# Kernel optimization log

Measured on AMD Instinct MI355X. Metric: run time of the kernel, lower is better.

Reference implementation:

```python
import jax, jax.numpy as jnp
import numpy as np

NB, C, N, H, W = 2, 128, 4, 64, 64
K = 9  # 3x3 kernel positions


def _conv(x, w, b, pad):
    y = jax.lax.conv_general_dilated(x, w, (1, 1), ((pad, pad), (pad, pad)),
                                     dimension_numbers=('NCHW', 'OIHW', 'NCHW'))
    return y + b[None, :, None, None]


def _bn(x, g, be, m, v, eps=1e-5):
    scale = g / jnp.sqrt(v + eps)
    return x * scale[None, :, None, None] + (be - m * scale)[None, :, None, None]


def _maxpool(x):
    # MaxPool2d(kernel_size=2, stride=1, padding=1): output H+1, W+1
    return jax.lax.reduce_window(x, -jnp.inf, jax.lax.max, (1, 1, 2, 2), (1, 1, 1, 1),
                                 ((0, 0), (0, 0), (1, 1), (1, 1)))


def _deform_conv(x, offset, mask, w, b):
    # modulated deformable conv v2, kernel 3x3, stride 1, padding 1
    n, c, h, wd = x.shape
    ky = jnp.repeat(jnp.arange(3), 3).astype(x.dtype)  # kernel row offsets
    kx = jnp.tile(jnp.arange(3), 3).astype(x.dtype)    # kernel col offsets
    dy = offset[:, 0::2]  # [n,K,h,w] (torchvision layout: interleaved dy,dx)
    dx = offset[:, 1::2]
    py = jnp.arange(h, dtype=x.dtype)[None, None, :, None] - 1.0 + ky[None, :, None, None] + dy
    px = jnp.arange(wd, dtype=x.dtype)[None, None, None, :] - 1.0 + kx[None, :, None, None] + dx
    y0 = jnp.floor(py)
    x0 = jnp.floor(px)
    wy = py - y0
    wx = px - x0
    xt = jnp.transpose(x, (0, 2, 3, 1))  # [n,h,w,c]
    bidx = jnp.arange(n)[:, None, None, None]

    def gather(yi, xi):
        valid = ((yi >= 0) & (yi < h) & (xi >= 0) & (xi < wd)).astype(x.dtype)
        yc = jnp.clip(yi, 0, h - 1).astype(jnp.int32)
        xc = jnp.clip(xi, 0, wd - 1).astype(jnp.int32)
        return xt[bidx, yc, xc] * valid[..., None]  # [n,K,h,w,c]

    v = (((1 - wy) * (1 - wx))[..., None] * gather(y0, x0)
         + ((1 - wy) * wx)[..., None] * gather(y0, x0 + 1)
         + (wy * (1 - wx))[..., None] * gather(y0 + 1, x0)
         + (wy * wx)[..., None] * gather(y0 + 1, x0 + 1))
    v = v * mask[..., None]  # modulation mask [n,K,h,w]
    out = jnp.einsum('nkhwc,ock->nohw', v, w.reshape(w.shape[0], c, K))
    return out + b[None, :, None, None]


def _forward(x, w1, b1, g1, be1, m1, v1, w_off, b_off, w_mod, b_mod, w_def, b_def,
             g2, be2, m2, v2, w_ds, b_ds, g3, be3, m3, v3):
    for i in range(NB):
        h = jax.nn.relu(_bn(_conv(x, w1[i], b1[i], 1), g1[i], be1[i], m1[i], v1[i]))
        off = _conv(h, w_off[i], b_off[i], 1)
        msk = 2.0 * jax.nn.sigmoid(_conv(h, w_mod[i], b_mod[i], 1))
        d = _bn(_deform_conv(h, off, msk, w_def[i], b_def[i]), g2[i], be2[i], m2[i], v2[i])
        res = _bn(_conv(x, w_ds[i], b_ds[i], 0), g3[i], be3[i], m3[i], v3[i])
        x = _maxpool(jax.nn.relu(d + res))
    return x


def setup_inputs() -> dict:
    key = jax.random.key(0)
    ks = iter(jax.random.split(key, 48))

    def rn(shape, s=0.05):
        return jax.random.normal(next(ks), shape, jnp.float32) * s

    def bnp():
        g = jax.random.uniform(next(ks), (NB, C), jnp.float32) * 0.5 + 0.75
        be = rn((NB, C), 0.1)
        m = rn((NB, C), 0.1)
        v = jax.random.uniform(next(ks), (NB, C), jnp.float32) * 0.5 + 0.75
        return g, be, m, v

    g1, be1, m1, v1 = bnp()
    g2, be2, m2, v2 = bnp()
    g3, be3, m3, v3 = bnp()
    return dict(
        x=jax.random.normal(next(ks), (N, C, H, W), jnp.float32),
        w1=rn((NB, C, C, 3, 3)), b1=rn((NB, C)),
        g1=g1, be1=be1, m1=m1, v1=v1,
        w_off=rn((NB, 2 * K, C, 3, 3), 0.01), b_off=rn((NB, 2 * K), 0.01),
        w_mod=rn((NB, K, C, 3, 3), 0.01), b_mod=rn((NB, K), 0.01),
        w_def=rn((NB, C, C, 3, 3)), b_def=rn((NB, C)),
        g2=g2, be2=be2, m2=m2, v2=v2,
        w_ds=rn((NB, C, C, 1, 1)), b_ds=rn((NB, C)),
        g3=g3, be3=be3, m3=m3, v3=v3,
    )


def reference(x, w1, b1, g1, be1, m1, v1, w_off, b_off, w_mod, b_mod, w_def, b_def,
              g2, be2, m2, v2, w_ds, b_ds, g3, be3, m3, v3):
    return _forward(x, w1, b1, g1, be1, m1, v1, w_off, b_off, w_mod, b_mod, w_def, b_def,
                    g2, be2, m2, v2, w_ds, b_ds, g3, be3, m3, v3)
```

## Files before the change

kernel.cpp:

```cpp
#include <hip/hip_runtime.h>
#include <math.h>

constexpr int NN = 4;
constexpr int CC = 128;

typedef unsigned short u16;
typedef short bfrag __attribute__((ext_vector_type(8)));
typedef float facc  __attribute__((ext_vector_type(4)));

__device__ __forceinline__ float bf2f(u16 v) {
    unsigned u = ((unsigned)v) << 16; float f; __builtin_memcpy(&f, &u, 4); return f;
}
__device__ __forceinline__ u16 f2bf(float f) {
    unsigned u; __builtin_memcpy(&u, &f, 4);
    unsigned r = u + 0x7FFFu + ((u >> 16) & 1u);
    return (u16)(r >> 16);
}

typedef const __attribute__((address_space(1))) unsigned int gu32;
typedef __attribute__((address_space(3))) unsigned int lu32;
__device__ __forceinline__ void gload16(const u16* g, u16* l) {
    __builtin_amdgcn_global_load_lds((gu32*)g, (lu32*)l, 16, 0, 0);
}

template<int WM, int WN, int MR, int NR, int NOB, int EPI>
__global__ __launch_bounds__(512)
void gconv_h(const u16* __restrict__ A, const u16* __restrict__ Wp,
             const float* __restrict__ bias, void* __restrict__ Out,
             int H, int W, int npb)
{
    constexpr int HALOW = 68;
    __shared__ __align__(16) u16 halo[4 * HALOW * 128];

    const int Hp = H + 2, Wq = W + 2, HW = H * W;
    const int tid = threadIdx.x, lane = tid & 63, wv = tid >> 6;
    const int wn = wv % WN, wm = wv / WN;
    const int colc = lane & 15, kg = lane >> 4;
    const int n = blockIdx.x / npb;
    const int pib = (blockIdx.x - n * npb) * 64;
    const int ymin = pib / W;

    {
        const u16* Abase = A + (size_t)n * Hp * Wq * 128;
        for (int c = wv; c < 4 * HALOW / 4; c += 8) {
            int o = c * 512 + lane * 8;
            int r = o / (HALOW * 128);
            int e = o - r * (HALOW * 128);
            int x = e >> 7;
            int g = (e >> 3) & 15;
            int xs = x < Wq ? x : Wq - 1;
            int pr = ymin + r; if (pr > Hp - 1) pr = Hp - 1;
            const u16* src = Abase + ((size_t)pr * Wq + xs) * 128 + (g ^ (x & 7)) * 8;
            gload16(src, &halo[c * 512]);
        }
    }
    __syncthreads();

    int dyr[MR], axr[MR];
#pragma unroll
    for (int r = 0; r < MR; ++r) {
        int m = wm * (MR * 16) + r * 16 + colc;
        int pixl = pib + m; if (pixl > HW - 1) pixl = HW - 1;
        int y = pixl / W;
        dyr[r] = y - ymin; axr[r] = pixl - y * W;
    }

    auto wfrag = [&](int tap, int cc, int q) -> const bfrag* {
        return (const bfrag*)(Wp + (size_t)tap * (NOB * 2048)
                              + ((cc * NOB + wn * NR + q) * 64 + lane) * 8);
    };

    bfrag bc[4][NR];
#pragma unroll
    for (int cc = 0; cc < 4; ++cc)
#pragma unroll
        for (int q = 0; q < NR; ++q) bc[cc][q] = *wfrag(0, cc, q);

    facc acc[MR][NR];
#pragma unroll
    for (int r = 0; r < MR; ++r)
#pragma unroll
        for (int q = 0; q < NR; ++q) acc[r][q] = (facc){0.f, 0.f, 0.f, 0.f};

#pragma unroll 1
    for (int t = 0; t < 9; ++t) {
        int ty = t / 3, tx = t - ty * 3;
        bfrag bn_[4][NR];
        if (t < 8) {
#pragma unroll
            for (int cc = 0; cc < 4; ++cc)
#pragma unroll
                for (int q = 0; q < NR; ++q) bn_[cc][q] = *wfrag(t + 1, cc, q);
        }
#pragma unroll
        for (int cc = 0; cc < 4; ++cc) {
            bfrag a[MR];
#pragma unroll
            for (int r = 0; r < MR; ++r) {
                int xx = axr[r] + tx;
                a[r] = *(const bfrag*)&halo[((dyr[r] + ty) * HALOW + xx) * 128
                                            + ((cc * 4 + kg) ^ (xx & 7)) * 8];
            }
#pragma unroll
            for (int r = 0; r < MR; ++r)
#pragma unroll
                for (int q = 0; q < NR; ++q)
                    acc[r][q] = __builtin_amdgcn_mfma_f32_16x16x32_bf16(a[r], bc[cc][q], acc[r][q], 0, 0, 0);
        }
        if (t < 8) {
#pragma unroll
            for (int cc = 0; cc < 4; ++cc)
#pragma unroll
                for (int q = 0; q < NR; ++q) bc[cc][q] = bn_[cc][q];
        }
    }

#pragma unroll
    for (int r = 0; r < MR; ++r) {
#pragma unroll
        for (int j = 0; j < 4; ++j) {
            int m = wm * (MR * 16) + r * 16 + kg * 4 + j;
            int pixl = pib + m;
            if (pixl >= HW) continue;
#pragma unroll
            for (int q = 0; q < NR; ++q) {
                int oc = wn * (NR * 16) + q * 16 + colc;
                float val = acc[r][q][j] + bias[oc];
                if constexpr (EPI == 0) {
                    val = fmaxf(val, 0.f);
                    int y = pixl / W, x = pixl - y * W;
                    ((u16*)Out)[((size_t)(n * Hp + y + 1) * Wq + x + 1) * 128 + oc] = f2bf(val);
                } else {
                    if (oc >= 18) val = 2.f / (1.f + expf(-val));
                    ((float*)Out)[((size_t)n * HW + pixl) * 32 + oc] = val;
                }
            }
        }
    }
}

__global__ __launch_bounds__(512, 4)
void deform7_k(const u16* __restrict__ Hb, const u16* __restrict__ Xp,
               const float* __restrict__ OM, const u16* __restrict__ Wp,
               const float* __restrict__ biasC, float* __restrict__ T,
               int H, int W, int tw, int th)
{
    __shared__ __align__(16) u16 halo[96 * 16 * 8];
    __shared__ __align__(16) u16 As3[3 * 32 * 128];
    __shared__ __align__(16) float oml[27 * 32];

    const int Hp = H + 2, Wq = W + 2, HW = H * W;
    const int tid = threadIdx.x, lane = tid & 63, wv = tid >> 6;
    const int wn = wv & 3, wm = wv >> 2;
    const int colc = lane & 15, kg = lane >> 4;
    int bt = blockIdx.x;
    int n = bt / (tw * th); int rt = bt - n * (tw * th);
    int ty0 = (rt / tw) * 4, tx0 = (rt - (rt / tw) * tw) * 8;
    const u16* Hbase = Hb + (size_t)n * Hp * Wq * 128;

#pragma unroll
    for (int c = 0; c < 3; ++c) {
        int g = c * 512 + tid;
        int s = g >> 4, u = g & 15;
        int row = s / 12, col = s - row * 12;
        int gy = min(max(ty0 - 2 + row, 0), H - 1);
        int gx = min(max(tx0 - 2 + col, 0), W - 1);
        int gr = u ^ (s & 15);
        gload16(Hbase + ((size_t)(gy + 1) * Wq + gx + 1) * 128 + gr * 8,
                &halo[(c * 512 + wv * 64) * 8]);
    }
    for (int e = tid; e < 27 * 32; e += 512) {
        int f = e >> 5, p = e & 31;
        int yy = min(ty0 + (p >> 3), H - 1), xx = min(tx0 + (p & 7), W - 1);
        oml[e] = OM[((size_t)n * HW + yy * W + xx) * 32 + f];
    }
    __syncthreads();

    const int g0 = tid & 15, m0 = (tid >> 4) & 31;
    const int cy1 = min(ty0 + (m0 >> 3), H - 1), cx1 = min(tx0 + (m0 & 7), W - 1);
    const int dslot = (g0 ^ (m0 & 7)) * 8;

    const int m = wm * 16 + colc;
    const int cyp = min(ty0 + (m >> 3), H - 1), cxp = min(tx0 + (m & 7), W - 1);
    const size_t xoff = ((size_t)(n * Hp + cyp + 1) * Wq + cxp + 1) * 128;

    auto wfrag = [&](int tap, int cc, int q) -> const bfrag* {
        return (const bfrag*)(Wp + (size_t)tap * 16384
                              + ((cc * 8 + wn * 2 + q) * 64 + lane) * 8);
    };

    auto sample1 = [&](int t, int tb) {
        float dy = oml[(2 * t) * 32 + m0];
        float dx = oml[(2 * t + 1) * 32 + m0];
        float mm = oml[(18 + t) * 32 + m0];
        float pyf = (float)cy1 - 1.f + (float)(t / 3) + dy;
        float pxf = (float)cx1 - 1.f + (float)(t % 3) + dx;
        float fy = floorf(pyf), fx = floorf(pxf);
        int y0 = (int)fy, x0 = (int)fx;
        float wy = pyf - fy, wx = pxf - fx;
        bool y0v = (y0 >= 0) && (y0 < H), y1v = (y0 >= -1) && (y0 < H - 1);
        bool x0v = (x0 >= 0) && (x0 < W), x1v = (x0 >= -1) && (x0 < W - 1);
        int yc0 = min(max(y0, 0), H - 1), yc1 = min(max(y0 + 1, 0), H - 1);
        int xc0 = min(max(x0, 0), W - 1), xc1 = min(max(x0 + 1, 0), W - 1);
        float w00 = (1.f - wy) * (1.f - wx) * ((y0v && x0v) ? mm : 0.f);
        float w01 = (1.f - wy) * wx         * ((y0v && x1v) ? mm : 0.f);
        float w10 = wy * (1.f - wx)         * ((y1v && x0v) ? mm : 0.f);
        float w11 = wy * wx                 * ((y1v && x1v) ? mm : 0.f);
        int ry0 = yc0 - ty0 + 2, ry1 = yc1 - ty0 + 2;
        int rx0 = xc0 - tx0 + 2, rx1 = xc1 - tx0 + 2;
        bool allin = (unsigned)ry0 < 8u && (unsigned)ry1 < 8u
                  && (unsigned)rx0 < 12u && (unsigned)rx1 < 12u;
        bfrag c00, c01, c10, c11;
        if (allin) {
            int s00 = ry0 * 12 + rx0, s01 = ry0 * 12 + rx1;
            int s10 = ry1 * 12 + rx0, s11 = ry1 * 12 + rx1;
            c00 = *(const bfrag*)&halo[(s00 * 16 + (g0 ^ (s00 & 15))) * 8];
            c01 = *(const bfrag*)&halo[(s01 * 16 + (g0 ^ (s01 & 15))) * 8];
            c10 = *(const bfrag*)&halo[(s10 * 16 + (g0 ^ (s10 & 15))) * 8];
            c11 = *(const bfrag*)&halo[(s11 * 16 + (g0 ^ (s11 & 15))) * 8];
        } else {
            c00 = *(const bfrag*)(Hbase + ((size_t)(yc0 + 1) * Wq + xc0 + 1) * 128 + g0 * 8);
            c01 = *(const bfrag*)(Hbase + ((size_t)(yc0 + 1) * Wq + xc1 + 1) * 128 + g0 * 8);
            c10 = *(const bfrag*)(Hbase + ((size_t)(yc1 + 1) * Wq + xc0 + 1) * 128 + g0 * 8);
            c11 = *(const bfrag*)(Hbase + ((size_t)(yc1 + 1) * Wq + xc1 + 1) * 128 + g0 * 8);
        }
        bfrag o;
#pragma unroll
        for (int j = 0; j < 8; ++j) {
            float f = w00 * bf2f((u16)c00[j]) + w01 * bf2f((u16)c01[j])
                    + w10 * bf2f((u16)c10[j]) + w11 * bf2f((u16)c11[j]);
            o[j] = (short)f2bf(f);
        }
        *(bfrag*)&As3[tb * 4096 + m0 * 128 + dslot] = o;
    };

    bfrag bc[4][2];
#pragma unroll
    for (int cc = 0; cc < 4; ++cc)
#pragma unroll
        for (int q = 0; q < 2; ++q) bc[cc][q] = *wfrag(0, cc, q);

    facc acc[2];
    acc[0] = (facc){0.f, 0.f, 0.f, 0.f};
    acc[1] = (facc){0.f, 0.f, 0.f, 0.f};

#pragma unroll 1
    for (int tg = 0; tg < 3; ++tg) {
        sample1(tg * 3 + 0, 0);
        sample1(tg * 3 + 1, 1);
        sample1(tg * 3 + 2, 2);
        __syncthreads();
#pragma unroll
        for (int tb = 0; tb < 3; ++tb) {
            int t = tg * 3 + tb;
            bfrag bn_[4][2];
#pragma unroll
            for (int cc = 0; cc < 4; ++cc)
#pragma unroll
                for (int q = 0; q < 2; ++q) bn_[cc][q] = *wfrag(t + 1, cc, q);
            const u16* as = &As3[tb * 4096];
#pragma unroll
            for (int cc = 0; cc < 4; ++cc) {
                bfrag a = *(const bfrag*)&as[m * 128 + ((cc * 4 + kg) ^ (m & 7)) * 8];
#pragma unroll
                for (int q = 0; q < 2; ++q)
                    acc[q] = __builtin_amdgcn_mfma_f32_16x16x32_bf16(a, bc[cc][q], acc[q], 0, 0, 0);
            }
#pragma unroll
            for (int cc = 0; cc < 4; ++cc)
#pragma unroll
                for (int q = 0; q < 2; ++q) bc[cc][q] = bn_[cc][q];
        }
        __syncthreads();
    }

#pragma unroll
    for (int cc = 0; cc < 4; ++cc) {
        bfrag a = *(const bfrag*)(Xp + xoff + (cc * 4 + kg) * 8);
#pragma unroll
        for (int q = 0; q < 2; ++q)
            acc[q] = __builtin_amdgcn_mfma_f32_16x16x32_bf16(a, bc[cc][q], acc[q], 0, 0, 0);
    }

#pragma unroll
    for (int j = 0; j < 4; ++j) {
        int mo = wm * 16 + kg * 4 + j;
        int y = ty0 + (mo >> 3), x = tx0 + (mo & 7);
        if (y >= H || x >= W) continue;
#pragma unroll
        for (int q = 0; q < 2; ++q) {
            int oc = wn * 32 + q * 16 + colc;
            T[((size_t)n * HW + y * W + x) * 128 + oc] = fmaxf(acc[q][j] + biasC[oc], 0.f);
        }
    }
}

template<int OUTMODE>
__global__ __launch_bounds__(256)
void pool_k(const float* __restrict__ T, void* __restrict__ Out, int H, int W)
{
    const int HW = H * W, Ho = H + 1, Wo = W + 1;
    int tot = NN * Ho * Wo * 16;
    int idx = blockIdx.x * 256 + threadIdx.x;
    if (idx >= tot) return;
    int cg = idx & 15; int t = idx >> 4;
    int ox = t % Wo; t /= Wo; int oy = t % Ho; int n = t / Ho;

    float mx[8];
#pragma unroll
    for (int j = 0; j < 8; ++j) mx[j] = -INFINITY;
#pragma unroll
    for (int d = 0; d < 2; ++d) {
        int iy = oy - 1 + d;
        if (iy < 0 || iy >= H) continue;
#pragma unroll
        for (int e = 0; e < 2; ++e) {
            int ix = ox - 1 + e;
            if (ix < 0 || ix >= W) continue;
            const float* src = T + ((size_t)(n * HW + iy * W + ix)) * 128 + cg * 8;
#pragma unroll
            for (int j = 0; j < 8; ++j) mx[j] = fmaxf(mx[j], src[j]);
        }
    }
    if constexpr (OUTMODE == 0) {
        int Hp2 = Ho + 2, Wp2 = Wo + 2;
        bfrag o;
#pragma unroll
        for (int j = 0; j < 8; ++j) o[j] = (short)f2bf(mx[j]);
        *(bfrag*)((u16*)Out + ((size_t)(n * Hp2 + oy + 1) * Wp2 + (ox + 1)) * 128 + cg * 8) = o;
    } else {
#pragma unroll
        for (int j = 0; j < 8; ++j) {
            int c = cg * 8 + j;
            ((float*)Out)[(((size_t)n * 128 + c) * Ho + oy) * Wo + ox] = mx[j];
        }
    }
}

__global__ __launch_bounds__(256)
void prolog_k(const float* __restrict__ x0,
              u16* __restrict__ Xp0, u16* __restrict__ Xp1,
              u16* __restrict__ Hp0, u16* __restrict__ Hp1,
              const float* __restrict__ w1, const float* __restrict__ b1,
              const float* __restrict__ g1, const float* __restrict__ be1,
              const float* __restrict__ m1, const float* __restrict__ v1,
              const float* __restrict__ w_off, const float* __restrict__ b_off,
              const float* __restrict__ w_mod, const float* __restrict__ b_mod,
              const float* __restrict__ w_def, const float* __restrict__ b_def,
              const float* __restrict__ g2, const float* __restrict__ be2,
              const float* __restrict__ m2, const float* __restrict__ v2,
              const float* __restrict__ w_ds, const float* __restrict__ b_ds,
              const float* __restrict__ g3, const float* __restrict__ be3,
              const float* __restrict__ m3, const float* __restrict__ v3,
              u16* __restrict__ Wb1p, u16* __restrict__ Wbomp, u16* __restrict__ Wbdp,
              float* __restrict__ bias1f, float* __restrict__ biasOM, float* __restrict__ biasC)
{
    const int P0 = 260, P1 = 264;
    const int B0 = NN * P0 * 16, B1 = NN * P1 * 16;
    int idx = blockIdx.x * 256 + threadIdx.x;
    bfrag z = (bfrag){0, 0, 0, 0, 0, 0, 0, 0};

    if (idx < 2 * B0) {
        u16* buf = idx < B0 ? Xp0 : Hp0;
        int e = idx < B0 ? idx : idx - B0;
        int gr = e & 15; int t = e >> 4;
        int b = t % P0; int n = t / P0;
        int y, x;
        if (b < 66)        { y = 0;  x = b; }
        else if (b < 132)  { y = 65; x = b - 66; }
        else { int r2 = b - 132; y = 1 + (r2 >> 1); x = (r2 & 1) ? 65 : 0; }
        *(bfrag*)(buf + ((size_t)(n * 66 + y) * 66 + x) * 128 + gr * 8) = z;
        return;
    }
    idx -= 2 * B0;
    if (idx < 2 * B1) {
        u16* buf = idx < B1 ? Xp1 : Hp1;
        int e = idx < B1 ? idx : idx - B1;
        int gr = e & 15; int t = e >> 4;
        int b = t % P1; int n = t / P1;
        int y, x;
        if (b < 67)        { y = 0;  x = b; }
        else if (b < 134)  { y = 66; x = b - 67; }
        else { int r2 = b - 134; y = 1 + (r2 >> 1); x = (r2 & 1) ? 66 : 0; }
        *(bfrag*)(buf + ((size_t)(n * 67 + y) * 67 + x) * 128 + gr * 8) = z;
        return;
    }
    idx -= 2 * B1;

    if (idx < NN * 64 * 64 * 16) {
        int cg = idx & 15; int t = idx >> 4;
        int x = t & 63; t >>= 6; int y = t & 63; int n = t >> 6;
        bfrag o;
#pragma unroll
        for (int j = 0; j < 8; ++j) {
            int c = cg * 8 + j;
            o[j] = (short)f2bf(x0[(((size_t)n * 128 + c) * 64 + y) * 64 + x]);
        }
        *(bfrag*)(Xp0 + ((size_t)(n * 66 + y + 1) * 66 + (x + 1)) * 128 + cg * 8) = o;
        return;
    }
    idx -= NN * 64 * 64 * 16;

    const int C1 = 9 * 4 * 8 * 512;
    const int C2 = 9 * 4 * 2 * 512;
    const int C3 = 10 * 4 * 8 * 512;
    if (idx < 2 * C1) {
        int inst = idx / C1, e = idx - inst * C1;
        int j = e & 7, lane = (e >> 3) & 63, rest = e >> 9;
        int ob = rest & 7; rest >>= 3; int cc = rest & 3; int tap = rest >> 2;
        int oc = ob * 16 + (lane & 15), c = cc * 32 + (lane >> 4) * 8 + j;
        float sc = g1[inst * 128 + oc] * rsqrtf(v1[inst * 128 + oc] + 1e-5f);
        Wb1p[idx] = f2bf(sc * w1[(((size_t)inst * 128 + oc) * 128 + c) * 9 + tap]);
        return;
    }
    idx -= 2 * C1;
    if (idx < 2 * C2) {
        int inst = idx / C2, e = idx - inst * C2;
        int j = e & 7, lane = (e >> 3) & 63, rest = e >> 9;
        int ob = rest & 1; rest >>= 1; int cc = rest & 3; int tap = rest >> 2;
        int oc = ob * 16 + (lane & 15), c = cc * 32 + (lane >> 4) * 8 + j;
        float v = 0.f;
        if (oc < 18)      v = w_off[(((size_t)inst * 18 + oc) * 128 + c) * 9 + tap];
        else if (oc < 27) v = w_mod[(((size_t)inst * 9 + (oc - 18)) * 128 + c) * 9 + tap];
        Wbomp[inst * C2 + e] = f2bf(v);
        return;
    }
    idx -= 2 * C2;
    if (idx < 2 * C3) {
        int inst = idx / C3, e = idx - inst * C3;
        int j = e & 7, lane = (e >> 3) & 63, rest = e >> 9;
        int ob = rest & 7; rest >>= 3; int cc = rest & 3; int tap = rest >> 2;
        int oc = ob * 16 + (lane & 15), c = cc * 32 + (lane >> 4) * 8 + j;
        float val;
        if (tap < 9) {
            float sc2 = g2[inst * 128 + oc] * rsqrtf(v2[inst * 128 + oc] + 1e-5f);
            val = sc2 * w_def[(((size_t)inst * 128 + oc) * 128 + c) * 9 + tap];
        } else {
            float sc3 = g3[inst * 128 + oc] * rsqrtf(v3[inst * 128 + oc] + 1e-5f);
            val = sc3 * w_ds[((size_t)inst * 128 + oc) * 128 + c];
        }
        Wbdp[inst * C3 + e] = f2bf(val);
        return;
    }
    idx -= 2 * C3;
    if (idx < 2 * 288) {
        int inst = idx / 288, r = idx - inst * 288;
        if (r < 128) {
            int oc = r, o = inst * 128 + oc;
            float sc = g1[o] * rsqrtf(v1[o] + 1e-5f);
            bias1f[o] = sc * b1[o] + be1[o] - m1[o] * sc;
        } else if (r < 160) {
            int oc = r - 128;
            float v = 0.f;
            if (oc < 18)      v = b_off[inst * 18 + oc];
            else if (oc < 27) v = b_mod[inst * 9 + (oc - 18)];
            biasOM[inst * 32 + oc] = v;
        } else {
            int oc = r - 160, o = inst * 128 + oc;
            float sc2 = g2[o] * rsqrtf(v2[o] + 1e-5f);
            float sc3 = g3[o] * rsqrtf(v3[o] + 1e-5f);
            biasC[o] = sc2 * b_def[o] + (be2[o] - m2[o] * sc2)
                     + sc3 * b_ds[o] + (be3[o] - m3[o] * sc3);
        }
    }
}

extern "C" void kernel_launch(void* const* d_in, const int* in_sizes, int n_in,
                              void* d_out, int out_size, void* d_ws, size_t ws_size,
                              hipStream_t stream)
{
    const float* x0    = (const float*)d_in[0];
    const float* w1    = (const float*)d_in[1];
    const float* b1    = (const float*)d_in[2];
    const float* g1    = (const float*)d_in[3];
    const float* be1   = (const float*)d_in[4];
    const float* m1    = (const float*)d_in[5];
    const float* v1    = (const float*)d_in[6];
    const float* w_off = (const float*)d_in[7];
    const float* b_off = (const float*)d_in[8];
    const float* w_mod = (const float*)d_in[9];
    const float* b_mod = (const float*)d_in[10];
    const float* w_def = (const float*)d_in[11];
    const float* b_def = (const float*)d_in[12];
    const float* g2    = (const float*)d_in[13];
    const float* be2   = (const float*)d_in[14];
    const float* m2    = (const float*)d_in[15];
    const float* v2    = (const float*)d_in[16];
    const float* w_ds  = (const float*)d_in[17];
    const float* b_ds  = (const float*)d_in[18];
    const float* g3    = (const float*)d_in[19];
    const float* be3   = (const float*)d_in[20];
    const float* m3    = (const float*)d_in[21];
    const float* v3    = (const float*)d_in[22];

    const int C1 = 147456, C2 = 36864, C3 = 163840;
    char* wsp = (char*)d_ws;
    auto alloc = [&](size_t bytes) { char* r = wsp; wsp += (bytes + 255) & ~(size_t)255; return r; };
    const size_t szX0 = (size_t)NN * 66 * 66 * 128 * 2;
    const size_t szX1 = (size_t)NN * 67 * 67 * 128 * 2;
    u16*   Xpad0  = (u16*)alloc(szX0);
    u16*   Xpad1  = (u16*)alloc(szX1);
    u16*   Hpad0  = (u16*)alloc(szX0);
    u16*   Hpad1  = (u16*)alloc(szX1);
    float* OFFMSK = (float*)alloc((size_t)16900 * 32 * 4);
    float* T      = (float*)alloc((size_t)16900 * 128 * 4);
    u16*   Wb1p   = (u16*)alloc((size_t)2 * C1 * 2);
    u16*   Wbomp  = (u16*)alloc((size_t)2 * C2 * 2);
    u16*   Wbdp   = (u16*)alloc((size_t)2 * C3 * 2);
    float* bias1f = (float*)alloc(2 * 128 * 4);
    float* biasOM = (float*)alloc(2 * 32 * 4);
    float* biasC  = (float*)alloc(2 * 128 * 4);

    const int B0 = NN * 260 * 16, B1 = NN * 264 * 16;
    int ptot = 2 * B0 + 2 * B1 + NN * 64 * 64 * 16 + 2 * C1 + 2 * C2 + 2 * C3 + 2 * 288;
    prolog_k<<<(ptot + 255) / 256, 256, 0, stream>>>(
        x0, Xpad0, Xpad1, Hpad0, Hpad1,
        w1, b1, g1, be1, m1, v1, w_off, b_off, w_mod, b_mod, w_def, b_def,
        g2, be2, m2, v2, w_ds, b_ds, g3, be3, m3, v3,
        Wb1p, Wbomp, Wbdp, bias1f, biasOM, biasC);

    const u16* curX = Xpad0;
    for (int i = 0; i < 2; ++i) {
        int H = 64 + i, W = 64 + i;
        int HW = H * W;
        int npb = (HW + 63) / 64;
        int grid = NN * npb;
        u16* Hpad = (i == 0) ? Hpad0 : Hpad1;

        gconv_h<2, 4, 2, 2, 8, 0><<<grid, 512, 0, stream>>>(
            curX, Wb1p + (size_t)i * C1, bias1f + i * 128, Hpad, H, W, npb);
        gconv_h<4, 2, 1, 1, 2, 1><<<grid, 512, 0, stream>>>(
            Hpad, Wbomp + (size_t)i * C2, biasOM + i * 32, OFFMSK, H, W, npb);
        int tw = (W + 7) / 8, th = (H + 3) / 4;
        deform7_k<<<NN * tw * th, 512, 0, stream>>>(
            Hpad, curX, OFFMSK, Wbdp + (size_t)i * C3, biasC + i * 128, T, H, W, tw, th);
        if (i == 0) {
            pool_k<0><<<(NN * 65 * 65 * 16 + 255) / 256, 256, 0, stream>>>(T, Xpad1, H, W);
        } else {
            pool_k<1><<<(NN * 66 * 66 * 16 + 255) / 256, 256, 0, stream>>>(T, d_out, H, W);
        }
        curX = Xpad1;
    }
}
```

Measured before the change: 136.9 us.

## Double-buffer deform sampling tiles and store intermediate in bf16

The deformable conv kernel now double-buffers its shared-memory A tiles, so bilinear sampling of the next tap group overlaps the MFMA work on the current group. Weight fragments are loaded inline rather than prefetched in registers. The intermediate T buffer between deform conv and maxpool is stored as bf16 instead of fp32, halving its write and read traffic. The costs are extra shared memory per block, which may reduce occupancy, and an extra bf16 rounding before the pool.

```diff
diff --git a/kernel.cpp b/kernel.cpp
--- a/kernel.cpp
+++ b/kernel.cpp
@@ -140,13 +140,13 @@
 }
 
 __global__ __launch_bounds__(512, 4)
-void deform7_k(const u16* __restrict__ Hb, const u16* __restrict__ Xp,
+void deform8_k(const u16* __restrict__ Hb, const u16* __restrict__ Xp,
                const float* __restrict__ OM, const u16* __restrict__ Wp,
-               const float* __restrict__ biasC, float* __restrict__ T,
+               const float* __restrict__ biasC, u16* __restrict__ T,
                int H, int W, int tw, int th)
 {
     __shared__ __align__(16) u16 halo[96 * 16 * 8];
-    __shared__ __align__(16) u16 As3[3 * 32 * 128];
+    __shared__ __align__(16) u16 As3[2][3 * 32 * 128];
     __shared__ __align__(16) float oml[27 * 32];
 
     const int Hp = H + 2, Wq = W + 2, HW = H * W;
@@ -184,12 +184,7 @@
     const int cyp = min(ty0 + (m >> 3), H - 1), cxp = min(tx0 + (m & 7), W - 1);
     const size_t xoff = ((size_t)(n * Hp + cyp + 1) * Wq + cxp + 1) * 128;
 
-    auto wfrag = [&](int tap, int cc, int q) -> const bfrag* {
-        return (const bfrag*)(Wp + (size_t)tap * 16384
-                              + ((cc * 8 + wn * 2 + q) * 64 + lane) * 8);
-    };
-
-    auto sample1 = [&](int t, int tb) {
+    auto sample1 = [&](int t, int buf, int tb) {
         float dy = oml[(2 * t) * 32 + m0];
         float dx = oml[(2 * t + 1) * 32 + m0];
         float mm = oml[(18 + t) * 32 + m0];
@@ -231,55 +226,52 @@
                     + w10 * bf2f((u16)c10[j]) + w11 * bf2f((u16)c11[j]);
             o[j] = (short)f2bf(f);
         }
-        *(bfrag*)&As3[tb * 4096 + m0 * 128 + dslot] = o;
+        *(bfrag*)&As3[buf][tb * 4096 + m0 * 128 + dslot] = o;
     };
 
-    bfrag bc[4][2];
-#pragma unroll
-    for (int cc = 0; cc < 4; ++cc)
-#pragma unroll
-        for (int q = 0; q < 2; ++q) bc[cc][q] = *wfrag(0, cc, q);
+    auto mfma3 = [&](int tg, int buf, facc* acc) {
+        const u16* as = As3[buf];
+#pragma unroll
+        for (int tb = 0; tb < 3; ++tb) {
+            int t = tg * 3 + tb;
+            const u16* wt = Wp + (size_t)t * 16384;
+#pragma unroll
+            for (int cc = 0; cc < 4; ++cc) {
+                bfrag a = *(const bfrag*)&as[tb * 4096 + m * 128 + ((cc * 4 + kg) ^ (m & 7)) * 8];
+#pragma unroll
+                for (int q = 0; q < 2; ++q) {
+                    bfrag b = *(const bfrag*)(wt + ((cc * 8 + wn * 2 + q) * 64 + lane) * 8);
+                    acc[q] = __builtin_amdgcn_mfma_f32_16x16x32_bf16(a, b, acc[q], 0, 0, 0);
+                }
+            }
+        }
+    };
 
     facc acc[2];
     acc[0] = (facc){0.f, 0.f, 0.f, 0.f};
     acc[1] = (facc){0.f, 0.f, 0.f, 0.f};
 
-#pragma unroll 1
-    for (int tg = 0; tg < 3; ++tg) {
-        sample1(tg * 3 + 0, 0);
-        sample1(tg * 3 + 1, 1);
-        sample1(tg * 3 + 2, 2);
-        __syncthreads();
-#pragma unroll
-        for (int tb = 0; tb < 3; ++tb) {
-            int t = tg * 3 + tb;
-            bfrag bn_[4][2];
-#pragma unroll
-            for (int cc = 0; cc < 4; ++cc)
-#pragma unroll
-                for (int q = 0; q < 2; ++q) bn_[cc][q] = *wfrag(t + 1, cc, q);
-            const u16* as = &As3[tb * 4096];
-#pragma unroll
-            for (int cc = 0; cc < 4; ++cc) {
-                bfrag a = *(const bfrag*)&as[m * 128 + ((cc * 4 + kg) ^ (m & 7)) * 8];
-#pragma unroll
-                for (int q = 0; q < 2; ++q)
-                    acc[q] = __builtin_amdgcn_mfma_f32_16x16x32_bf16(a, bc[cc][q], acc[q], 0, 0, 0);
+    sample1(0, 0, 0); sample1(1, 0, 1); sample1(2, 0, 2);
+    __syncthreads();
+    sample1(3, 1, 0); sample1(4, 1, 1); sample1(5, 1, 2);
+    mfma3(0, 0, acc);
+    __syncthreads();
+    sample1(6, 0, 0); sample1(7, 0, 1); sample1(8, 0, 2);
+    mfma3(1, 1, acc);
+    __syncthreads();
+    mfma3(2, 0, acc);
+
+    {
+        const u16* wt = Wp + (size_t)9 * 16384;
+#pragma unroll
+        for (int cc = 0; cc < 4; ++cc) {
+            bfrag a = *(const bfrag*)(Xp + xoff + (cc * 4 + kg) * 8);
+#pragma unroll
+            for (int q = 0; q < 2; ++q) {
+                bfrag b = *(const bfrag*)(wt + ((cc * 8 + wn * 2 + q) * 64 + lane) * 8);
+                acc[q] = __builtin_amdgcn_mfma_f32_16x16x32_bf16(a, b, acc[q], 0, 0, 0);
             }
-#pragma unroll
-            for (int cc = 0; cc < 4; ++cc)
-#pragma unroll
-                for (int q = 0; q < 2; ++q) bc[cc][q] = bn_[cc][q];
-        }
-        __syncthreads();
-    }
-
-#pragma unroll
-    for (int cc = 0; cc < 4; ++cc) {
-        bfrag a = *(const bfrag*)(Xp + xoff + (cc * 4 + kg) * 8);
-#pragma unroll
-        for (int q = 0; q < 2; ++q)
-            acc[q] = __builtin_amdgcn_mfma_f32_16x16x32_bf16(a, bc[cc][q], acc[q], 0, 0, 0);
+        }
     }
 
 #pragma unroll
@@ -290,14 +282,15 @@
 #pragma unroll
         for (int q = 0; q < 2; ++q) {
             int oc = wn * 32 + q * 16 + colc;
-            T[((size_t)n * HW + y * W + x) * 128 + oc] = fmaxf(acc[q][j] + biasC[oc], 0.f);
+            T[((size_t)n * HW + y * W + x) * 128 + oc] =
+                f2bf(fmaxf(acc[q][j] + biasC[oc], 0.f));
         }
     }
 }
 
 template<int OUTMODE>
 __global__ __launch_bounds__(256)
-void pool_k(const float* __restrict__ T, void* __restrict__ Out, int H, int W)
+void pool_k(const u16* __restrict__ T, void* __restrict__ Out, int H, int W)
 {
     const int HW = H * W, Ho = H + 1, Wo = W + 1;
     int tot = NN * Ho * Wo * 16;
@@ -317,9 +310,9 @@
         for (int e = 0; e < 2; ++e) {
             int ix = ox - 1 + e;
             if (ix < 0 || ix >= W) continue;
-            const float* src = T + ((size_t)(n * HW + iy * W + ix)) * 128 + cg * 8;
-#pragma unroll
-            for (int j = 0; j < 8; ++j) mx[j] = fmaxf(mx[j], src[j]);
+            bfrag v = *(const bfrag*)(T + ((size_t)(n * HW + iy * W + ix)) * 128 + cg * 8);
+#pragma unroll
+            for (int j = 0; j < 8; ++j) mx[j] = fmaxf(mx[j], bf2f((u16)v[j]));
         }
     }
     if constexpr (OUTMODE == 0) {
@@ -503,7 +496,7 @@
     u16*   Hpad0  = (u16*)alloc(szX0);
     u16*   Hpad1  = (u16*)alloc(szX1);
     float* OFFMSK = (float*)alloc((size_t)16900 * 32 * 4);
-    float* T      = (float*)alloc((size_t)16900 * 128 * 4);
+    u16*   T      = (u16*)alloc((size_t)16900 * 128 * 2);
     u16*   Wb1p   = (u16*)alloc((size_t)2 * C1 * 2);
     u16*   Wbomp  = (u16*)alloc((size_t)2 * C2 * 2);
     u16*   Wbdp   = (u16*)alloc((size_t)2 * C3 * 2);
@@ -532,7 +525,7 @@
         gconv_h<4, 2, 1, 1, 2, 1><<<grid, 512, 0, stream>>>(
             Hpad, Wbomp + (size_t)i * C2, biasOM + i * 32, OFFMSK, H, W, npb);
         int tw = (W + 7) / 8, th = (H + 3) / 4;
-        deform7_k<<<NN * tw * th, 512, 0, stream>>>(
+        deform8_k<<<NN * tw * th, 512, 0, stream>>>(
             Hpad, curX, OFFMSK, Wbdp + (size_t)i * C3, biasC + i * 128, T, H, W, tw, th);
         if (i == 0) {
             pool_k<0><<<(NN * 65 * 65 * 16 + 255) / 256, 256, 0, stream>>>(T, Xpad1, H, W);
```

Result: faster. 132.3 us (-3.4%).
